# Optimization experiments

Measured on AMD Instinct MI355X. Metric: run time of the kernel, lower is better.

The kernel has to match this reference:

```python
import jax, jax.numpy as jnp
import numpy as np
import math

B, S, H, NH = 1, 2048, 1024, 16  # batch, seq, hidden, heads


def setup_inputs() -> dict:
    key = jax.random.key(0)
    ks = jax.random.split(key, 12)
    inp = {
        "query": jax.random.normal(ks[0], (B, S, H), dtype=jnp.float32),
        "key": jax.random.normal(ks[1], (B, S, H), dtype=jnp.float32),
        "value": jax.random.normal(ks[2], (B, S, H), dtype=jnp.float32),
        "attention_mask": jax.random.randint(ks[3], (1, 1, S, S), 0, 2, dtype=jnp.int32),
        # torch nn.Linear params: y = x @ W.T + b, W init ~ U(-1/sqrt(H), 1/sqrt(H))
        "Wq": jax.random.uniform(ks[4], (H, H), jnp.float32, -1, 1) / math.sqrt(H),
        "bq": jax.random.uniform(ks[5], (H,), jnp.float32, -1, 1) / math.sqrt(H),
        "Wk": jax.random.uniform(ks[6], (H, H), jnp.float32, -1, 1) / math.sqrt(H),
        "bk": jax.random.uniform(ks[7], (H,), jnp.float32, -1, 1) / math.sqrt(H),
        "Wv": jax.random.uniform(ks[8], (H, H), jnp.float32, -1, 1) / math.sqrt(H),
        "bv": jax.random.uniform(ks[9], (H,), jnp.float32, -1, 1) / math.sqrt(H),
        "Wo": jax.random.uniform(ks[10], (H, H), jnp.float32, -1, 1) / math.sqrt(H),
        "bo": jax.random.uniform(ks[11], (H,), jnp.float32, -1, 1) / math.sqrt(H),
        "head": NH,
        "hidden_size": H,
    }
    return inp


def reference(query, key, value, attention_mask, Wq, bq, Wk, bk, Wv, bv, Wo, bo, head, hidden_size):
    b, s, _ = query.shape
    d_k = hidden_size // head

    def proj(x, W, bias):
        # [b, s, hidden] -> [b, head, s, d_k]
        y = x @ W.T + bias
        return y.reshape(b, s, head, d_k).transpose(0, 2, 1, 3)

    q = proj(query, Wq, bq)
    k = proj(key, Wk, bk)
    v = proj(value, Wv, bv)

    # naive full score matrix, as in the source (scale by sqrt(d_k) = last dim of q)
    scores = jnp.einsum("bhqd,bhkd->bhqk", q, k) / math.sqrt(d_k)
    # faithful quirk: masked positions are set to 0 (not -inf) before softmax
    scores = jnp.where(attention_mask == 0, jnp.zeros((), scores.dtype), scores)
    attn = jax.nn.softmax(scores, axis=-1)

    out = jnp.einsum("bhqk,bhkd->bhqd", attn, v)  # [b, head, s, d_k]
    out = out.transpose(0, 2, 1, 3).reshape(b, s, head * d_k)
    return out @ Wo.T + bo
```

## Files before the change

### kernel.cpp

```cpp
#include <hip/hip_runtime.h>
#include <hip/hip_bf16.h>


#define S_LEN 2048
#define HID   1024
#define NHEAD 16
#define DK    64

typedef unsigned short u16;
typedef __attribute__((ext_vector_type(8))) short bf16x8;
typedef __attribute__((ext_vector_type(4))) short bf16x4;
typedef __attribute__((ext_vector_type(4))) float f32x4;
typedef __attribute__((ext_vector_type(2))) unsigned u32x2;
typedef __attribute__((ext_vector_type(4))) unsigned u32x4;

__device__ __forceinline__ void load16_lds(const void* g, void* l) {
  __builtin_amdgcn_global_load_lds(
      (const __attribute__((address_space(1))) void*)g,
      (__attribute__((address_space(3))) void*)l, 16, 0, 0);
}

__device__ __forceinline__ short bfbits(float x) {
  __hip_bfloat16 h = __float2bfloat16(x);
  return *(short*)&h;
}
__device__ __forceinline__ bf16x8 cvt8(float4 a, float4 b) {
  bf16x8 r;
  r[0] = bfbits(a.x); r[1] = bfbits(a.y); r[2] = bfbits(a.z); r[3] = bfbits(a.w);
  r[4] = bfbits(b.x); r[5] = bfbits(b.y); r[6] = bfbits(b.z); r[7] = bfbits(b.w);
  return r;
}
__device__ __forceinline__ float bf2f(u16 u) {
  unsigned v = (unsigned)u << 16;
  return *(float*)&v;
}

__global__ __launch_bounds__(256) void cvt_pack_kernel(
    const float* __restrict__ q, const float* __restrict__ k,
    const float* __restrict__ v, const float* __restrict__ wq,
    const float* __restrict__ wk, const float* __restrict__ wv,
    const float* __restrict__ wo, const int* __restrict__ mask,
    u16* __restrict__ Xbf, u16* __restrict__ Wbf,
    unsigned int* __restrict__ bits) {
  const int y = blockIdx.y;
  if (y == 7) {
    if (blockIdx.x >= 512) return;
    int idx = blockIdx.x * 256 + threadIdx.x;
    const int4* p = (const int4*)(mask + (size_t)idx * 32);
    unsigned word = 0;
#pragma unroll
    for (int i = 0; i < 8; ++i) {
      int4 mv = p[i];
      word |= (unsigned)(mv.x != 0) << (i * 4 + 0);
      word |= (unsigned)(mv.y != 0) << (i * 4 + 1);
      word |= (unsigned)(mv.z != 0) << (i * 4 + 2);
      word |= (unsigned)(mv.w != 0) << (i * 4 + 3);
    }
    bits[idx] = word;
    return;
  }
  size_t i = ((size_t)blockIdx.x * 256 + threadIdx.x) * 8;
  const float* src;
  u16* dst;
  size_t n;
  if (y < 3) {
    src = y == 0 ? q : (y == 1 ? k : v);
    dst = Xbf + (size_t)y * (S_LEN * HID);
    n = (size_t)S_LEN * HID;
  } else {
    int w = y - 3;
    src = w == 0 ? wq : (w == 1 ? wk : (w == 2 ? wv : wo));
    dst = Wbf + (size_t)w * (HID * HID);
    n = (size_t)HID * HID;
  }
  if (i >= n) return;
  float4 a = *(const float4*)(src + i);
  float4 b = *(const float4*)(src + i + 4);
  *(bf16x8*)(dst + i) = cvt8(a, b);
}

__global__ __launch_bounds__(256, 3) void gemm_qkv(
    const u16* __restrict__ Xbf, const u16* __restrict__ Wbf,
    const float* __restrict__ bq, const float* __restrict__ bk,
    const float* __restrict__ bv, u16* __restrict__ Qb,
    u16* __restrict__ Kb, u16* __restrict__ Vt) {
  constexpr int Mm = 2048, Kk = 1024, NIT = 16;
  const int tid = threadIdx.x, lane = tid & 63, wave = tid >> 6;
  const int q4 = lane >> 4, c16 = lane & 15;
  const int bx = blockIdx.x;
  const int xcd = bx & 7, s = bx >> 3;
  const int mh = s / 24;
  const int mBase = ((xcd >> 1) * 4 + mh) * 128;
  const int nG = (xcd & 1) * 24 + (s - mh * 24);
  const int nBase = nG * 64;
  const int z = nBase >> 10;
  const u16* A = Xbf + (size_t)z * (S_LEN * HID);
  const float* bias = z == 0 ? bq : (z == 1 ? bk : bv);
  const float oscale = (z == 0) ? 0.125f * 1.44269504088896f : 1.0f;

  const int wr = wave >> 1, wc = wave & 1;

  __shared__ __align__(16) u16 As[2][2][128 * 32];
  __shared__ __align__(16) u16 Bs[2][2][64 * 32];

  f32x4 acc[4][2] = {};
  const int srow = lane >> 2;
  const int sx8 = ((lane & 3) ^ ((srow >> 1) & 3)) * 8;
  const int rx8 = (q4 ^ ((c16 >> 1) & 3)) * 8;

  auto issue = [&](int it, int buf) {
#pragma unroll
    for (int j = 0; j < 4; ++j) {
      int u = wave * 4 + j, h = u >> 3, grp = u & 7;
      load16_lds(A + (size_t)(mBase + grp * 16 + srow) * Kk + it * 64 +
                     h * 32 + sx8,
                 &As[buf][h][grp * 512]);
    }
#pragma unroll
    for (int j = 0; j < 2; ++j) {
      int u = wave * 2 + j, h = u >> 2, grp = u & 3;
      int brow = grp * 16 + srow;
      int b32 = brow & 31;
      int bsrc = (brow & 32) | ((b32 & 15) * 2 + (b32 >> 4));
      load16_lds(Wbf + (size_t)(nBase + bsrc) * Kk + it * 64 +
                     h * 32 + sx8,
                 &Bs[buf][h][grp * 512]);
    }
  };

  issue(0, 0);
  __syncthreads();

  for (int it = 0; it < NIT; ++it) {
    const int buf = it & 1, nbuf = buf ^ 1;
    if (it + 1 < NIT) issue(it + 1, nbuf);
#pragma unroll
    for (int kk = 0; kk < 2; ++kk) {
      bf16x8 af[4], bfr[2];
#pragma unroll
      for (int t = 0; t < 4; ++t)
        af[t] = *(const bf16x8*)&As[buf][kk][(wr * 64 + t * 16 + c16) * 32 + rx8];
#pragma unroll
      for (int t = 0; t < 2; ++t)
        bfr[t] = *(const bf16x8*)&Bs[buf][kk][(wc * 32 + t * 16 + c16) * 32 + rx8];
#pragma unroll
      for (int mt = 0; mt < 4; ++mt)
#pragma unroll
        for (int nt = 0; nt < 2; ++nt)
          acc[mt][nt] = __builtin_amdgcn_mfma_f32_16x16x32_bf16(
              af[mt], bfr[nt], acc[mt][nt], 0, 0, 0);
    }
    __syncthreads();
  }

  const int colE = wc * 32 + c16 * 2;
  if (z == 2) {
    u16* LT = (u16*)&As[0][0][0];
#pragma unroll
    for (int nt = 0; nt < 2; ++nt) {
      int col = colE + nt;
      float bv2 = bias[((nBase & 1023) + col)];
#pragma unroll
      for (int mt = 0; mt < 4; ++mt) {
        int row0 = wr * 64 + mt * 16 + q4 * 4;
        int vv0 = row0 & 31;
        int rowp0 = (row0 & ~31) | (((vv0 & 15) >> 2) << 3) |
                    (((vv0 >> 4) & 1) << 2);
        bf16x4 t;
#pragma unroll
        for (int r = 0; r < 4; ++r) t[r] = bfbits(acc[mt][nt][r] + bv2);
        *(bf16x4*)&LT[col * 132 + rowp0] = t;
      }
    }
    __syncthreads();
#pragma unroll
    for (int rep = 0; rep < 4; ++rep) {
      int u = rep * 256 + tid;
      int col = u >> 4, seg = u & 15;
      bf16x8 vvv = *(const bf16x8*)&LT[col * 132 + seg * 8];
      *(bf16x8*)(Vt + (size_t)((nBase & 1023) + col) * Mm + mBase + seg * 8) = vvv;
    }
  } else {
    u16* C = z == 0 ? Qb : Kb;
    int colg = (nBase & 1023) + colE;
    float2 b2 = *(const float2*)&bias[colg];
#pragma unroll
    for (int mt = 0; mt < 4; ++mt) {
#pragma unroll
      for (int r = 0; r < 4; ++r) {
        int row = mBase + wr * 64 + mt * 16 + q4 * 4 + r;
        float v0 = (acc[mt][0][r] + b2.x) * oscale;
        float v1 = (acc[mt][1][r] + b2.y) * oscale;
        unsigned pk;
        asm("v_cvt_pk_bf16_f32 %0, %1, %2" : "=v"(pk) : "v"(v0), "v"(v1));
        *(unsigned*)&C[(size_t)row * 1024 + colg] = pk;
      }
    }
  }
}

__global__ __launch_bounds__(512, 4) void attn_kernel(
    const u16* __restrict__ Qb, const u16* __restrict__ Kb,
    const u16* __restrict__ Vt, const unsigned* __restrict__ mb,
    u16* __restrict__ partOA, u16* __restrict__ partO3,
    float* __restrict__ partL) {
  constexpr int NITA = 8;
  const int lin = blockIdx.x + 8 * (blockIdx.y + 16 * blockIdx.z);
  const int work = ((lin & 7) << 6) | (lin >> 3);
  const int qt = work & 7, h = (work >> 3) & 15, zz = work >> 7;
  const int tid = threadIdx.x, lane = tid & 63, wave = tid >> 6;
  const int q4 = lane >> 4, c16 = lane & 15;

  __shared__ __align__(16) u16 Ks[2][2][64 * 32];
  __shared__ __align__(16) u16 Vs[2][2][64 * 32];

  const int q0 = qt * 256 + wave * 32;

  bf16x8 qf[2][2];
#pragma unroll
  for (int m = 0; m < 2; ++m)
#pragma unroll
    for (int kk = 0; kk < 2; ++kk)
      qf[m][kk] = *(const bf16x8*)(Qb + (size_t)(q0 + m * 16 + c16) * HID +
                                   h * DK + kk * 32 + q4 * 8);

  f32x4 o[2][4] = {};
  float l_lane[2] = {0.0f, 0.0f};

  const int srow = lane >> 2;
  const int sx8 = ((lane & 3) ^ ((srow >> 1) & 3)) * 8;
  const int rx8 = (q4 ^ ((c16 >> 1) & 3)) * 8;
  const int kvbase = zz * (S_LEN / 4);

  auto issueKV = [&](int it, int buf) {
    const int kv0 = kvbase + it * 64;
#pragma unroll
    for (int j = 0; j < 2; ++j) {
      int i = wave * 2 + j;
      if (i < 8) {
        int half = i >> 2, grp = i & 3;
        load16_lds(Kb + (size_t)(kv0 + grp * 16 + srow) * HID + h * DK +
                       half * 32 + sx8,
                   &Ks[buf][half][grp * 512]);
      } else {
        int ii = i - 8;
        int half = ii >> 2, grp = ii & 3;
        load16_lds(Vt + (size_t)(h * DK + grp * 16 + srow) * S_LEN + kv0 +
                       half * 32 + sx8,
                   &Vs[buf][half][grp * 512]);
      }
    }
  };

  issueKV(0, 0);
  __syncthreads();

  for (int it = 0; it < NITA; ++it) {
    const int buf = it & 1, nbuf = buf ^ 1;
    if (it + 1 < NITA) issueKV(it + 1, nbuf);

    u32x2 mw[2];
#pragma unroll
    for (int m = 0; m < 2; ++m)
      mw[m] = *(const u32x2*)(mb + (size_t)(q0 + m * 16 + c16) * 64 +
                              (kvbase >> 5) + it * 2);

#pragma unroll
    for (int kk = 0; kk < 2; ++kk) {
      f32x4 sv[2][2];
      __builtin_amdgcn_s_setprio(1);
#pragma unroll
      for (int ntb = 0; ntb < 2; ++ntb) {
        const int nt = kk * 2 + ntb;
        const int rsw = (nt * 16 + c16) * 32 + rx8;
        bf16x8 kf0 = *(const bf16x8*)&Ks[buf][0][rsw];
        bf16x8 kf1 = *(const bf16x8*)&Ks[buf][1][rsw];
#pragma unroll
        for (int m = 0; m < 2; ++m) {
          f32x4 a = {};
          a = __builtin_amdgcn_mfma_f32_16x16x32_bf16(kf0, qf[m][0], a, 0, 0, 0);
          a = __builtin_amdgcn_mfma_f32_16x16x32_bf16(kf1, qf[m][1], a, 0, 0, 0);
          sv[m][ntb] = a;
        }
      }
      __builtin_amdgcn_s_setprio(0);

      bf16x8 pa[2];
#pragma unroll
      for (int m = 0; m < 2; ++m) {
        const unsigned word = kk ? mw[m][1] : mw[m][0];
        float p[8];
#pragma unroll
        for (int ntb = 0; ntb < 2; ++ntb)
#pragma unroll
          for (int r = 0; r < 4; ++r) {
            const int bit = ntb * 16 + q4 * 4 + r;
            float s = ((word >> bit) & 1u) ? sv[m][ntb][r] : 0.0f;
            float e;
            asm("v_exp_f32 %0, %1" : "=v"(e) : "v"(s));
            l_lane[m] += e;
            p[ntb * 4 + r] = e;
          }
        u32x4 pk;
#pragma unroll
        for (int j = 0; j < 4; ++j)
          asm("v_cvt_pk_bf16_f32 %0, %1, %2"
              : "=v"(pk[j]) : "v"(p[2 * j]), "v"(p[2 * j + 1]));
        pa[m] = *(bf16x8*)&pk;
      }

      __builtin_amdgcn_s_setprio(1);
#pragma unroll
      for (int ntv = 0; ntv < 4; ++ntv) {
        const int rsw = (ntv * 16 + c16) * 32 + rx8;
        bf16x8 vb = *(const bf16x8*)&Vs[buf][kk][rsw];
        o[0][ntv] = __builtin_amdgcn_mfma_f32_16x16x32_bf16(pa[0], vb, o[0][ntv], 0, 0, 0);
        o[1][ntv] = __builtin_amdgcn_mfma_f32_16x16x32_bf16(pa[1], vb, o[1][ntv], 0, 0, 0);
      }
      __builtin_amdgcn_s_setprio(0);
    }
    __syncthreads();
  }

  u16* pO = (zz < 3) ? (partOA + (size_t)zz * (S_LEN * HID)) : partO3;
#pragma unroll
  for (int m = 0; m < 2; ++m) {
    float s = l_lane[m];
    s += __shfl_xor(s, 16);
    s += __shfl_xor(s, 32);
    int qrow = q0 + m * 16 + c16;
    if (q4 == 0)
      partL[((size_t)zz * NHEAD + h) * S_LEN + qrow] = s;
#pragma unroll
    for (int r = 0; r < 4; ++r) {
      int row = q0 + m * 16 + q4 * 4 + r;
#pragma unroll
      for (int nt = 0; nt < 4; ++nt)
        ((__hip_bfloat16*)pO)[(size_t)row * HID + h * DK + nt * 16 + c16] =
            __float2bfloat16(o[m][nt][r]);
    }
  }
}

__global__ __launch_bounds__(256) void gemm_out(
    const u16* __restrict__ pOA, const u16* __restrict__ pO3,
    const float* __restrict__ partL, const u16* __restrict__ Wo,
    const float* __restrict__ bo, float* __restrict__ out) {
  constexpr int Nn = 1024, Kk = 1024, NIT = 16;
  constexpr size_t M2 = (size_t)S_LEN * HID;
  const int tid = threadIdx.x, lane = tid & 63, wave = tid >> 6;
  const int q4 = lane >> 4, c16 = lane & 15;
  const int bx = blockIdx.x;
  const int xcd = bx & 7, s = bx >> 3;
  const int mBase = (xcd * 8 + (s & 7)) * 32;
  const int nBase = (s >> 3) * 128;
  const int wn = wave * 32;

  __shared__ __align__(16) u16 As[2][2][32 * 32];
  __shared__ __align__(16) u16 Bs[2][2][128 * 32];
  __shared__ float linv[32][16];

  f32x4 acc[2][2] = {};
  const int srow = lane >> 2;
  const int sx8 = ((lane & 3) ^ ((srow >> 1) & 3)) * 8;
  const int rx8 = (q4 ^ ((c16 >> 1) & 3)) * 8;

  const int arow = tid >> 3, acu = tid & 7;
  const int ahalf = acu >> 2;
  const int aoff = arow * 32 + ((acu & 3) ^ ((arow >> 1) & 3)) * 8;

  auto issueB = [&](int it, int buf) {
#pragma unroll
    for (int j = 0; j < 4; ++j) {
      int u = wave * 4 + j, h = u >> 3, grp = u & 7;
      load16_lds(Wo + (size_t)(nBase + grp * 16 + srow) * Kk + it * 64 +
                     h * 32 + sx8,
                 &Bs[buf][h][grp * 512]);
    }
  };

  bf16x8 avA[4], avB[4];
  auto aloadTo = [&](bf16x8* dst, int it) {
    const u16* p = pOA + (size_t)(mBase + arow) * Kk + it * 64 + acu * 8;
    dst[0] = *(const bf16x8*)p;
    dst[1] = *(const bf16x8*)(p + M2);
    dst[2] = *(const bf16x8*)(p + 2 * M2);
    dst[3] = *(const bf16x8*)(pO3 + (size_t)(mBase + arow) * Kk + it * 64 + acu * 8);
  };
  auto awriteFrom = [&](const bf16x8* src, int it, int buf) {
    float inv = linv[arow][it];
    bf16x8 r;
#pragma unroll
    for (int j = 0; j < 8; ++j) {
      float v = (bf2f((u16)src[0][j]) + bf2f((u16)src[1][j]) +
                 bf2f((u16)src[2][j]) + bf2f((u16)src[3][j])) * inv;
      r[j] = bfbits(v);
    }
    *(bf16x8*)&As[buf][ahalf][aoff] = r;
  };

#pragma unroll
  for (int e = 0; e < 2; ++e) {
    int idx = tid * 2 + e, row = idx >> 4, hh = idx & 15;
    float l = 0.0f;
#pragma unroll
    for (int z = 0; z < 4; ++z)
      l += partL[(size_t)(z * NHEAD + hh) * S_LEN + mBase + row];
    linv[row][hh] = 1.0f / l;
  }
  aloadTo(avA, 0);
  issueB(0, 0);
  __syncthreads();
  awriteFrom(avA, 0, 0);
  aloadTo(avB, 1);
  __syncthreads();

  for (int it = 0; it < NIT; ++it) {
    const int buf = it & 1, nbuf = buf ^ 1;
    if (it + 1 < NIT) issueB(it + 1, nbuf);
    if (it + 2 < NIT) aloadTo((it & 1) ? avB : avA, it + 2);
#pragma unroll
    for (int kk = 0; kk < 2; ++kk) {
      bf16x8 af[2], bfr[2];
#pragma unroll
      for (int t = 0; t < 2; ++t)
        af[t] = *(const bf16x8*)&As[buf][kk][(t * 16 + c16) * 32 + rx8];
#pragma unroll
      for (int t = 0; t < 2; ++t)
        bfr[t] = *(const bf16x8*)&Bs[buf][kk][(wn + t * 16 + c16) * 32 + rx8];
#pragma unroll
      for (int mt = 0; mt < 2; ++mt)
#pragma unroll
        for (int nt = 0; nt < 2; ++nt)
          acc[mt][nt] = __builtin_amdgcn_mfma_f32_16x16x32_bf16(
              af[mt], bfr[nt], acc[mt][nt], 0, 0, 0);
    }
    if (it + 1 < NIT) awriteFrom((it & 1) ? avA : avB, it + 1, nbuf);
    __syncthreads();
  }

#pragma unroll
  for (int nt = 0; nt < 2; ++nt) {
    int col = nBase + wn + nt * 16 + c16;
    float bv = bo[col];
#pragma unroll
    for (int mt = 0; mt < 2; ++mt)
#pragma unroll
      for (int r = 0; r < 4; ++r) {
        int row = mBase + mt * 16 + q4 * 4 + r;
        out[(size_t)row * Nn + col] = acc[mt][nt][r] + bv;
      }
  }
}

extern "C" void kernel_launch(void* const* d_in, const int* in_sizes, int n_in,
                              void* d_out, int out_size, void* d_ws, size_t ws_size,
                              hipStream_t stream) {
  const float* q    = (const float*)d_in[0];
  const float* k    = (const float*)d_in[1];
  const float* v    = (const float*)d_in[2];
  const int*   mask = (const int*)d_in[3];
  const float* Wq = (const float*)d_in[4];
  const float* bq = (const float*)d_in[5];
  const float* Wk = (const float*)d_in[6];
  const float* bk = (const float*)d_in[7];
  const float* Wv = (const float*)d_in[8];
  const float* bv = (const float*)d_in[9];
  const float* Wo = (const float*)d_in[10];
  const float* bo = (const float*)d_in[11];

  const size_t M2 = (size_t)S_LEN * HID;
  const size_t W1 = (size_t)HID * HID;
  const size_t need = (4 * W1 + 3 * M2 + 3 * M2) * 2 +
                      (size_t)S_LEN * 64 * 4 + 2 * NHEAD * S_LEN * 4;
  if (ws_size < need) return;

  u16* Wbf = (u16*)d_ws;
  u16* Xbf = Wbf + 4 * W1;
  u16* Qb = Xbf + 3 * M2;
  u16* Kb = Qb + M2;
  u16* Vt = Kb + M2;
  unsigned* mbits = (unsigned*)(Vt + M2);
  u16* partOA = Xbf;
  u16* partO3 = Wbf;
  float* partL = (float*)(Wbf + 2 * W1);

  hipLaunchKernelGGL(cvt_pack_kernel, dim3(1024, 8), dim3(256), 0, stream,
                     q, k, v, Wq, Wk, Wv, Wo, mask, Xbf, Wbf, mbits);

  hipLaunchKernelGGL(gemm_qkv, dim3(768), dim3(256), 0, stream,
                     Xbf, Wbf, bq, bk, bv, Qb, Kb, Vt);

  hipLaunchKernelGGL(attn_kernel, dim3(S_LEN / 256, NHEAD, 4), dim3(512), 0,
                     stream, Qb, Kb, Vt, mbits, partOA, partO3, partL);

  hipLaunchKernelGGL(gemm_out, dim3(512), dim3(256), 0, stream,
                     partOA, partO3, partL, Wbf + 3 * W1, bo, (float*)d_out);
}
```

Before: 188.9 us.

## Fuse fp32-to-bf16 activation conversion into QKV GEMM A-tile loads

After: 199.4 us. 1.06x slower.

```diff
diff --git a/kernel.cpp b/kernel.cpp
--- a/kernel.cpp
+++ b/kernel.cpp
@@ -36,14 +36,12 @@
 }
 
 __global__ __launch_bounds__(256) void cvt_pack_kernel(
-    const float* __restrict__ q, const float* __restrict__ k,
-    const float* __restrict__ v, const float* __restrict__ wq,
-    const float* __restrict__ wk, const float* __restrict__ wv,
-    const float* __restrict__ wo, const int* __restrict__ mask,
-    u16* __restrict__ Xbf, u16* __restrict__ Wbf,
+    const float* __restrict__ wq, const float* __restrict__ wk,
+    const float* __restrict__ wv, const float* __restrict__ wo,
+    const int* __restrict__ mask, u16* __restrict__ Wbf,
     unsigned int* __restrict__ bits) {
   const int y = blockIdx.y;
-  if (y == 7) {
+  if (y == 4) {
     if (blockIdx.x >= 512) return;
     int idx = blockIdx.x * 256 + threadIdx.x;
     const int4* p = (const int4*)(mask + (size_t)idx * 32);
@@ -59,28 +57,18 @@
     bits[idx] = word;
     return;
   }
+  if (blockIdx.x >= 512) return;
   size_t i = ((size_t)blockIdx.x * 256 + threadIdx.x) * 8;
-  const float* src;
-  u16* dst;
-  size_t n;
-  if (y < 3) {
-    src = y == 0 ? q : (y == 1 ? k : v);
-    dst = Xbf + (size_t)y * (S_LEN * HID);
-    n = (size_t)S_LEN * HID;
-  } else {
-    int w = y - 3;
-    src = w == 0 ? wq : (w == 1 ? wk : (w == 2 ? wv : wo));
-    dst = Wbf + (size_t)w * (HID * HID);
-    n = (size_t)HID * HID;
-  }
-  if (i >= n) return;
+  const float* src = y == 0 ? wq : (y == 1 ? wk : (y == 2 ? wv : wo));
+  u16* dst = Wbf + (size_t)y * (HID * HID);
   float4 a = *(const float4*)(src + i);
   float4 b = *(const float4*)(src + i + 4);
   *(bf16x8*)(dst + i) = cvt8(a, b);
 }
 
 __global__ __launch_bounds__(256, 3) void gemm_qkv(
-    const u16* __restrict__ Xbf, const u16* __restrict__ Wbf,
+    const float* __restrict__ qx, const float* __restrict__ kx,
+    const float* __restrict__ vx, const u16* __restrict__ Wbf,
     const float* __restrict__ bq, const float* __restrict__ bk,
     const float* __restrict__ bv, u16* __restrict__ Qb,
     u16* __restrict__ Kb, u16* __restrict__ Vt) {
@@ -94,7 +82,7 @@
   const int nG = (xcd & 1) * 24 + (s - mh * 24);
   const int nBase = nG * 64;
   const int z = nBase >> 10;
-  const u16* A = Xbf + (size_t)z * (S_LEN * HID);
+  const float* Araw = z == 0 ? qx : (z == 1 ? kx : vx);
   const float* bias = z == 0 ? bq : (z == 1 ? bk : bv);
   const float oscale = (z == 0) ? 0.125f * 1.44269504088896f : 1.0f;
 
@@ -108,14 +96,26 @@
   const int sx8 = ((lane & 3) ^ ((srow >> 1) & 3)) * 8;
   const int rx8 = (q4 ^ ((c16 >> 1) & 3)) * 8;
 
-  auto issue = [&](int it, int buf) {
+  float4 ar[4][2];
+  auto aload = [&](int it) {
 #pragma unroll
     for (int j = 0; j < 4; ++j) {
       int u = wave * 4 + j, h = u >> 3, grp = u & 7;
-      load16_lds(A + (size_t)(mBase + grp * 16 + srow) * Kk + it * 64 +
-                     h * 32 + sx8,
-                 &As[buf][h][grp * 512]);
-    }
+      const float* p = Araw + (size_t)(mBase + grp * 16 + srow) * Kk +
+                       it * 64 + h * 32 + sx8;
+      ar[j][0] = *(const float4*)p;
+      ar[j][1] = *(const float4*)(p + 4);
+    }
+  };
+  auto awrite = [&](int buf) {
+#pragma unroll
+    for (int j = 0; j < 4; ++j) {
+      int u = wave * 4 + j, h = u >> 3, grp = u & 7;
+      *(bf16x8*)&As[buf][h][grp * 512 + lane * 8] = cvt8(ar[j][0], ar[j][1]);
+    }
+  };
+
+  auto issueB = [&](int it, int buf) {
 #pragma unroll
     for (int j = 0; j < 2; ++j) {
       int u = wave * 2 + j, h = u >> 2, grp = u & 3;
@@ -128,12 +128,14 @@
     }
   };
 
-  issue(0, 0);
+  aload(0);
+  issueB(0, 0);
+  awrite(0);
   __syncthreads();
 
   for (int it = 0; it < NIT; ++it) {
     const int buf = it & 1, nbuf = buf ^ 1;
-    if (it + 1 < NIT) issue(it + 1, nbuf);
+    if (it + 1 < NIT) { aload(it + 1); issueB(it + 1, nbuf); }
 #pragma unroll
     for (int kk = 0; kk < 2; ++kk) {
       bf16x8 af[4], bfr[2];
@@ -150,6 +152,7 @@
           acc[mt][nt] = __builtin_amdgcn_mfma_f32_16x16x32_bf16(
               af[mt], bfr[nt], acc[mt][nt], 0, 0, 0);
     }
+    if (it + 1 < NIT) awrite(nbuf);
     __syncthreads();
   }
 
@@ -476,20 +479,20 @@
   if (ws_size < need) return;
 
   u16* Wbf = (u16*)d_ws;
-  u16* Xbf = Wbf + 4 * W1;
-  u16* Qb = Xbf + 3 * M2;
+  u16* Xscr = Wbf + 4 * W1;
+  u16* Qb = Xscr + 3 * M2;
   u16* Kb = Qb + M2;
   u16* Vt = Kb + M2;
   unsigned* mbits = (unsigned*)(Vt + M2);
-  u16* partOA = Xbf;
+  u16* partOA = Xscr;
   u16* partO3 = Wbf;
   float* partL = (float*)(Wbf + 2 * W1);
 
-  hipLaunchKernelGGL(cvt_pack_kernel, dim3(1024, 8), dim3(256), 0, stream,
-                     q, k, v, Wq, Wk, Wv, Wo, mask, Xbf, Wbf, mbits);
+  hipLaunchKernelGGL(cvt_pack_kernel, dim3(1024, 5), dim3(256), 0, stream,
+                     Wq, Wk, Wv, Wo, mask, Wbf, mbits);
 
   hipLaunchKernelGGL(gemm_qkv, dim3(768), dim3(256), 0, stream,
-                     Xbf, Wbf, bq, bk, bv, Qb, Kb, Vt);
+                     q, k, v, Wbf, bq, bk, bv, Qb, Kb, Vt);
 
   hipLaunchKernelGGL(attn_kernel, dim3(S_LEN / 256, NHEAD, 4), dim3(512), 0,
                      stream, Qb, Kb, Vt, mbits, partOA, partO3, partL);
```
